# Kernel optimization log

Measured on AMD Instinct MI355X. Metric: run time of the kernel, lower is better.

## Reference

```python
import jax, jax.numpy as jnp
import numpy as np

N_NODES = 100000


def _gcn_conv(x, edge_index, W, b, n_nodes):
    # PyG GCNConv with add_self_loops=True, default gcn_norm:
    #   out = D^{-1/2} (A + I) D^{-1/2} (x @ W) + b
    xw = x @ W  # [N, out_dim]
    src = jnp.concatenate([edge_index[0], jnp.arange(n_nodes)])
    dst = jnp.concatenate([edge_index[1], jnp.arange(n_nodes)])
    ones = jnp.ones(src.shape[0], dtype=x.dtype)
    deg = jax.ops.segment_sum(ones, dst, num_segments=n_nodes)  # includes self loops
    dinv = jnp.where(deg > 0, jax.lax.rsqrt(deg), 0.0)
    norm = dinv[src] * dinv[dst]  # [E + N]
    msgs = xw[src] * norm[:, None]  # gather + scale per edge
    out = jax.ops.segment_sum(msgs, dst, num_segments=n_nodes)
    return out + b


def setup_inputs() -> dict:
    key = jax.random.key(0)
    k1, k2, k3, k4 = jax.random.split(key, 4)
    N, E = N_NODES, 1600000
    in_dim, hid_dim, out_dim = 128, 128, 64
    x = jax.random.normal(k1, (N, in_dim), dtype=jnp.float32)
    edge_index = jax.random.randint(k2, (2, E), 0, N, dtype=jnp.int64)
    W1 = jax.random.normal(k3, (in_dim, hid_dim), dtype=jnp.float32) * (1.0 / np.sqrt(in_dim))
    b1 = jnp.zeros((hid_dim,), dtype=jnp.float32)
    W2 = jax.random.normal(k4, (hid_dim, out_dim), dtype=jnp.float32) * (1.0 / np.sqrt(hid_dim))
    b2 = jnp.zeros((out_dim,), dtype=jnp.float32)
    return {"x": x, "edge_index": edge_index, "W1": W1, "b1": b1, "W2": W2, "b2": b2}


def reference(x, edge_index, W1, b1, W2, b2):
    h = _gcn_conv(x, edge_index, W1, b1, N_NODES)
    out = _gcn_conv(h, edge_index, W2, b2, N_NODES)
    return out
```

## Files before the change

### kernel.cpp

```cpp
#include <hip/hip_runtime.h>

#define NNODES 100000
#define NBUCK ((NNODES + 127) >> 7)
#define CAPB 3072
#define BINCAP 16
#define GFILL 256

typedef __attribute__((ext_vector_type(8))) short short8;
typedef __attribute__((ext_vector_type(4))) float f32x4;

__device__ __forceinline__ float bf2f(unsigned short u) {
    unsigned int v = ((unsigned int)u) << 16;
    return __builtin_bit_cast(float, v);
}
__device__ __forceinline__ unsigned short f2bf(float f) {
    unsigned int u = __builtin_bit_cast(unsigned int, f);
    u += 0x7FFF + ((u >> 16) & 1);
    return (unsigned short)(u >> 16);
}


__global__ __launch_bounds__(512) void fill_wc(const int* __restrict__ ei, int E,
                                               int* __restrict__ gcur,
                                               int* __restrict__ seg) {
    __shared__ int lcnt[NBUCK];
    __shared__ int lbin[NBUCK * BINCAP];

    const int t = threadIdx.x;
    for (int i = t; i < NBUCK; i += 512) lcnt[i] = 0;
    __syncthreads();

    const int per = (E + GFILL - 1) / GFILL;
    const int e0 = blockIdx.x * per;
    const int e1 = min(e0 + per, E);

    for (int base = e0; base < e1; base += 512) {
        int e = base + t;
        if (e < e1) {
            int src = ei[e];
            int d = ei[E + e];
            int b = (unsigned)d >> 7;
            int p = (src << 7) | (d & 127);
            int pos = atomicAdd(&lcnt[b], 1);
            if (pos < BINCAP) {
                lbin[b * BINCAP + pos] = p;
            } else {
                int gp = atomicAdd(&gcur[b << 4], 1);
                if (gp < CAPB) seg[b * CAPB + gp] = p;
            }
        }
        __syncthreads();
        for (int bb = t; bb < NBUCK; bb += 512) {
            if (lcnt[bb] >= BINCAP) {
                int gp = atomicAdd(&gcur[bb << 4], BINCAP);
                if (gp + BINCAP <= CAPB) {
                    int* dp = seg + bb * CAPB + gp;
                    const int* sp = lbin + bb * BINCAP;
#pragma unroll
                    for (int j = 0; j < BINCAP; ++j) dp[j] = sp[j];
                }
                lcnt[bb] = 0;
            }
        }
        __syncthreads();
    }
    for (int bb = t; bb < NBUCK; bb += 512) {
        int c = min(lcnt[bb], BINCAP);
        if (c > 0) {
            int gp = atomicAdd(&gcur[bb << 4], c);
            int* dp = seg + bb * CAPB;
            const int* sp = lbin + bb * BINCAP;
            for (int j = 0; j < c && gp + j < CAPB; ++j) dp[gp + j] = sp[j];
        }
    }
}


__global__ __launch_bounds__(512) void sortseg(const int* __restrict__ gcur,
                                               int* __restrict__ seg,
                                               float* __restrict__ dinv,
                                               int* __restrict__ rsb,
                                               int* __restrict__ cntb, int N) {
    __shared__ int el[CAPB];
    __shared__ int csr[CAPB];
    __shared__ int cnt[128], sh[128], rs[128], cur[128];

    const int t = threadIdx.x, b = blockIdx.x;
    const int total = min(gcur[b << 4], CAPB);

    if (t < 128) cnt[t] = 0;
    __syncthreads();
    {
        const int* sp = seg + b * CAPB;
        for (int i = t; i < total; i += 512) el[i] = sp[i];
    }
    __syncthreads();

    for (int i = t; i < total; i += 512) atomicAdd(&cnt[el[i] & 127], 1);
    __syncthreads();
    int v = (t < 128) ? cnt[t] : 0;
    if (t < 128) sh[t] = v;
    __syncthreads();
    for (int offp = 1; offp < 128; offp <<= 1) {
        int u = (t < 128 && t >= offp) ? sh[t - offp] : 0;
        __syncthreads();
        if (t < 128) sh[t] += u;
        __syncthreads();
    }
    if (t < 128) {
        int excl = sh[t] - v;
        rs[t] = excl;
        cur[t] = excl;
    }
    __syncthreads();
    for (int i = t; i < total; i += 512) {
        int p = el[i];
        int pos = atomicAdd(&cur[p & 127], 1);
        csr[pos] = (int)((unsigned)p >> 7);
    }
    __syncthreads();

    {
        int* dp = seg + b * CAPB;
        for (int i = t; i < total; i += 512) dp[i] = csr[i];
    }
    if (t < 128) {
        rsb[b * 128 + t] = rs[t];
        cntb[b * 128 + t] = cnt[t];
        int node = (b << 7) + t;
        if (node < N) dinv[node] = rsqrtf((float)cnt[t] + 1.0f);
    }
}


__global__ __launch_bounds__(256) void w12_kernel(const float* __restrict__ W1,
                                                  const float* __restrict__ b1,
                                                  const float* __restrict__ W2,
                                                  float* __restrict__ W12,
                                                  float* __restrict__ bW2,
                                                  unsigned short* __restrict__ whi,
                                                  unsigned short* __restrict__ wlo) {
    int j = threadIdx.x % 64;
    int r = threadIdx.x / 64;
    if (blockIdx.x < 32) {
        int i = blockIdx.x * 4 + r;
        float acc = 0.f;
        for (int k = 0; k < 128; ++k) acc += W1[i * 128 + k] * W2[k * 64 + j];
        W12[i * 64 + j] = acc;
        int kc = i >> 5;
        int ik = i & 31;
        int lane = ((ik >> 3) << 4) | (j & 15);
        int jj = ik & 7;
        int nt = j >> 4;
        size_t idx = (size_t)(((nt << 2) | kc) * 64 + lane) * 8 + jj;
        unsigned short h = f2bf(acc);
        whi[idx] = h;
        wlo[idx] = f2bf(acc - bf2f(h));
    } else if (r == 0) {
        float acc = 0.f;
        for (int k = 0; k < 128; ++k) acc += b1[k] * W2[k * 64 + j];
        bW2[j] = acc;
    }
}


__global__ __launch_bounds__(256) void gemm_mfma(const float* __restrict__ X,
                                                 const unsigned short* __restrict__ whi,
                                                 const unsigned short* __restrict__ wlo,
                                                 const float* __restrict__ dinv,
                                                 unsigned short* __restrict__ Ybf, int N) {
    const int tid = threadIdx.x;
    const int wv = tid >> 6;
    const int l = tid & 63;
    const int lm = l & 15;
    const int lk = l >> 4;
    const int rowbase = blockIdx.x * 64 + wv * 16;
    const int arow = min(rowbase + lm, N - 1);

    const float* xp = X + (size_t)arow * 128 + lk * 8;

    f32x4 acc[4];
#pragma unroll
    for (int nt = 0; nt < 4; ++nt) acc[nt] = (f32x4){0.f, 0.f, 0.f, 0.f};

#pragma unroll
    for (int kc = 0; kc < 4; ++kc) {
        float4 xa = *(const float4*)(xp + kc * 32);
        float4 xb = *(const float4*)(xp + kc * 32 + 4);
        float xs[8] = {xa.x, xa.y, xa.z, xa.w, xb.x, xb.y, xb.z, xb.w};
        short8 ah, al;
#pragma unroll
        for (int j = 0; j < 8; ++j) {
            unsigned short h = f2bf(xs[j]);
            ah[j] = (short)h;
            al[j] = (short)f2bf(xs[j] - bf2f(h));
        }
#pragma unroll
        for (int nt = 0; nt < 4; ++nt) {
            const size_t fb = (size_t)(((nt << 2) | kc) * 64 + l) * 8;
            short8 bh = *(const short8*)(whi + fb);
            short8 bl = *(const short8*)(wlo + fb);
            acc[nt] = __builtin_amdgcn_mfma_f32_16x16x32_bf16(ah, bh, acc[nt], 0, 0, 0);
            acc[nt] = __builtin_amdgcn_mfma_f32_16x16x32_bf16(ah, bl, acc[nt], 0, 0, 0);
            acc[nt] = __builtin_amdgcn_mfma_f32_16x16x32_bf16(al, bh, acc[nt], 0, 0, 0);
        }
    }

#pragma unroll
    for (int i = 0; i < 4; ++i) {
        int r = rowbase + lk * 4 + i;
        if (r < N) {
            float dv = dinv[r];
#pragma unroll
            for (int nt = 0; nt < 4; ++nt)
                Ybf[(size_t)r * 64 + nt * 16 + lm] = f2bf(acc[nt][i] * dv);
        }
    }
}


template <bool FINAL>
__global__ __launch_bounds__(256, 8) void agg_csr(const int* __restrict__ seg,
                                                  const int* __restrict__ rsb,
                                                  const int* __restrict__ cntb,
                                                  const unsigned short* __restrict__ Y,
                                                  const float* __restrict__ dinv,
                                                  const float* __restrict__ bW2,
                                                  const float* __restrict__ b2,
                                                  unsigned short* __restrict__ out_bf,
                                                  float* __restrict__ out_f, int N) {
    __shared__ int csrS[CAPB];
    __shared__ int rsS[32], cntS[32];

    const int t = threadIdx.x;
    const int b = blockIdx.x >> 2;
    const int q = blockIdx.x & 3;
    const int nb = q << 5;

    if (t < 32) {
        rsS[t] = rsb[b * 128 + nb + t];
        cntS[t] = cntb[b * 128 + nb + t];
    }
    __syncthreads();
    const int start = rsS[0];
    const int L = rsS[31] + cntS[31] - start;
    {
        const int* sp = seg + (size_t)b * CAPB + start;
        for (int i = t; i < L; i += 256) csrS[i] = sp[i];
    }
    __syncthreads();

    const int g = t >> 3, lane = t & 7, c8 = lane * 8;
    const int node = (b << 7) + nb + g;
    if (node >= N) return;

    float a[8];
    {
        short8 sv = *(const short8*)(Y + (size_t)node * 64 + c8);
#pragma unroll
        for (int j = 0; j < 8; ++j) a[j] = bf2f((unsigned short)sv[j]);
    }
    float ds = 0.f;

    const int s0 = rsS[g] - start;
    const int ne = cntS[g];
    const int e0 = s0 + ne;
    int i = s0;

    for (; i + 8 <= e0; i += 8) {
        int a0 = csrS[i + 0];
        int a1 = csrS[i + 1];
        int a2 = csrS[i + 2];
        int a3 = csrS[i + 3];
        int a4 = csrS[i + 4];
        int a5 = csrS[i + 5];
        int a6 = csrS[i + 6];
        int a7 = csrS[i + 7];
        short8 v0 = *(const short8*)(Y + (size_t)a0 * 64 + c8);
        short8 v1 = *(const short8*)(Y + (size_t)a1 * 64 + c8);
        short8 v2 = *(const short8*)(Y + (size_t)a2 * 64 + c8);
        short8 v3 = *(const short8*)(Y + (size_t)a3 * 64 + c8);
        short8 v4 = *(const short8*)(Y + (size_t)a4 * 64 + c8);
        short8 v5 = *(const short8*)(Y + (size_t)a5 * 64 + c8);
        short8 v6 = *(const short8*)(Y + (size_t)a6 * 64 + c8);
        short8 v7 = *(const short8*)(Y + (size_t)a7 * 64 + c8);
        if (FINAL) ds += dinv[csrS[i + lane]];
#pragma unroll
        for (int j = 0; j < 8; ++j) {
            a[j] += bf2f((unsigned short)v0[j]) + bf2f((unsigned short)v1[j])
                  + bf2f((unsigned short)v2[j]) + bf2f((unsigned short)v3[j])
                  + bf2f((unsigned short)v4[j]) + bf2f((unsigned short)v5[j])
                  + bf2f((unsigned short)v6[j]) + bf2f((unsigned short)v7[j]);
        }
    }
    for (; i + 4 <= e0; i += 4) {
        int a0 = csrS[i + 0];
        int a1 = csrS[i + 1];
        int a2 = csrS[i + 2];
        int a3 = csrS[i + 3];
        short8 v0 = *(const short8*)(Y + (size_t)a0 * 64 + c8);
        short8 v1 = *(const short8*)(Y + (size_t)a1 * 64 + c8);
        short8 v2 = *(const short8*)(Y + (size_t)a2 * 64 + c8);
        short8 v3 = *(const short8*)(Y + (size_t)a3 * 64 + c8);
        if (FINAL && lane < 4) ds += dinv[csrS[i + lane]];
#pragma unroll
        for (int j = 0; j < 8; ++j) {
            a[j] += bf2f((unsigned short)v0[j]) + bf2f((unsigned short)v1[j])
                  + bf2f((unsigned short)v2[j]) + bf2f((unsigned short)v3[j]);
        }
    }
    for (; i < e0; ++i) {
        int aa = csrS[i];
        short8 vv = *(const short8*)(Y + (size_t)aa * 64 + c8);
        if (FINAL && lane == 0) ds += dinv[aa];
#pragma unroll
        for (int j = 0; j < 8; ++j) a[j] += bf2f((unsigned short)vv[j]);
    }

    float di = rsqrtf((float)ne + 1.0f);
    if (FINAL) {
        float dt = ds;
        dt += __shfl_xor(dt, 1, 64);
        dt += __shfl_xor(dt, 2, 64);
        dt += __shfl_xor(dt, 4, 64);
        float si = di * (di + dt);
        float4 bb0 = *(const float4*)(bW2 + c8);
        float4 bb1 = *(const float4*)(bW2 + c8 + 4);
        float4 bv0 = *(const float4*)(b2 + c8);
        float4 bv1 = *(const float4*)(b2 + c8 + 4);
        float4 o0, o1;
        o0.x = di * a[0] + si * bb0.x + bv0.x;
        o0.y = di * a[1] + si * bb0.y + bv0.y;
        o0.z = di * a[2] + si * bb0.z + bv0.z;
        o0.w = di * a[3] + si * bb0.w + bv0.w;
        o1.x = di * a[4] + si * bb1.x + bv1.x;
        o1.y = di * a[5] + si * bb1.y + bv1.y;
        o1.z = di * a[6] + si * bb1.z + bv1.z;
        o1.w = di * a[7] + si * bb1.w + bv1.w;
        *(float4*)(out_f + (size_t)node * 64 + c8) = o0;
        *(float4*)(out_f + (size_t)node * 64 + c8 + 4) = o1;
    } else {
        float d2 = di * di;
        short8 o;
#pragma unroll
        for (int j = 0; j < 8; ++j) o[j] = (short)f2bf(d2 * a[j]);
        *(short8*)(out_bf + (size_t)node * 64 + c8) = o;
    }
}


extern "C" void kernel_launch(void* const* d_in, const int* in_sizes, int n_in,
                              void* d_out, int out_size, void* d_ws, size_t ws_size,
                              hipStream_t stream) {
    const float* x  = (const float*)d_in[0];
    const int*   ei = (const int*)d_in[1];
    const float* W1 = (const float*)d_in[2];
    const float* b1 = (const float*)d_in[3];
    const float* W2 = (const float*)d_in[4];
    const float* b2 = (const float*)d_in[5];
    float* out = (float*)d_out;

    const int N = NNODES;
    const int E = in_sizes[1] / 2;

    float* ws   = (float*)d_ws;
    float* dinv = ws;
    float* W12  = dinv + N;
    float* bW2  = W12 + 8192;
    unsigned short* whi = (unsigned short*)(bW2 + 64);
    unsigned short* wlo = whi + 8192;
    unsigned short* ybf = wlo + 8192;
    unsigned short* zbf = ybf + (size_t)N * 64;
    int*  seg  = (int*)(zbf + (size_t)N * 64);
    int*  gcur = seg + (size_t)NBUCK * CAPB;
    int*  rsb  = gcur + (size_t)NBUCK * 16;
    int*  cntb = rsb + (size_t)NBUCK * 128;

    hipMemsetAsync(gcur, 0, (size_t)NBUCK * 16 * sizeof(int), stream);

    fill_wc<<<GFILL, 512, 0, stream>>>(ei, E, gcur, seg);
    w12_kernel<<<33, 256, 0, stream>>>(W1, b1, W2, W12, bW2, whi, wlo);
    sortseg<<<NBUCK, 512, 0, stream>>>(gcur, seg, dinv, rsb, cntb, N);

    gemm_mfma<<<(N + 63) / 64, 256, 0, stream>>>(x, whi, wlo, dinv, ybf, N);
    agg_csr<false><<<NBUCK * 4, 256, 0, stream>>>(seg, rsb, cntb, ybf, dinv, nullptr, nullptr, zbf, nullptr, N);
    agg_csr<true><<<NBUCK * 4, 256, 0, stream>>>(seg, rsb, cntb, zbf, dinv, bW2, b2, nullptr, out, N);
}
```

Measured before the change: 211.1 us.

## Fuse bucket sort into first aggregation and compute degrees with global atomics

Removes the separate sortseg kernel. Node degrees are now counted with global atomics inside fill_wc. Each first-layer aggregation block (one quarter of a 128-node bucket) scans the whole bucket segment, filters the entries for its 32 nodes, and scatters them into a local CSR, which it writes out for reuse by the second layer. This saves a launch and the separate sort pass, but each bucket segment is read four times, fill_wc gains global atomics, and dinv is recomputed from deg in several places.

Result: slower. 263.7 us (+24.9%).

```diff
diff --git a/kernel.cpp b/kernel.cpp
--- a/kernel.cpp
+++ b/kernel.cpp
@@ -3,6 +3,7 @@
 #define NNODES 100000
 #define NBUCK ((NNODES + 127) >> 7)
 #define CAPB 3072
+#define QCAP 1024
 #define BINCAP 16
 #define GFILL 256
 
@@ -22,7 +23,8 @@
 
 __global__ __launch_bounds__(512) void fill_wc(const int* __restrict__ ei, int E,
                                                int* __restrict__ gcur,
-                                               int* __restrict__ seg) {
+                                               int* __restrict__ seg,
+                                               int* __restrict__ deg) {
     __shared__ int lcnt[NBUCK];
     __shared__ int lbin[NBUCK * BINCAP];
 
@@ -39,6 +41,7 @@
         if (e < e1) {
             int src = ei[e];
             int d = ei[E + e];
+            atomicAdd(&deg[d], 1);
             int b = (unsigned)d >> 7;
             int p = (src << 7) | (d & 127);
             int pos = atomicAdd(&lcnt[b], 1);
@@ -72,63 +75,6 @@
             const int* sp = lbin + bb * BINCAP;
             for (int j = 0; j < c && gp + j < CAPB; ++j) dp[gp + j] = sp[j];
         }
-    }
-}
-
-
-__global__ __launch_bounds__(512) void sortseg(const int* __restrict__ gcur,
-                                               int* __restrict__ seg,
-                                               float* __restrict__ dinv,
-                                               int* __restrict__ rsb,
-                                               int* __restrict__ cntb, int N) {
-    __shared__ int el[CAPB];
-    __shared__ int csr[CAPB];
-    __shared__ int cnt[128], sh[128], rs[128], cur[128];
-
-    const int t = threadIdx.x, b = blockIdx.x;
-    const int total = min(gcur[b << 4], CAPB);
-
-    if (t < 128) cnt[t] = 0;
-    __syncthreads();
-    {
-        const int* sp = seg + b * CAPB;
-        for (int i = t; i < total; i += 512) el[i] = sp[i];
-    }
-    __syncthreads();
-
-    for (int i = t; i < total; i += 512) atomicAdd(&cnt[el[i] & 127], 1);
-    __syncthreads();
-    int v = (t < 128) ? cnt[t] : 0;
-    if (t < 128) sh[t] = v;
-    __syncthreads();
-    for (int offp = 1; offp < 128; offp <<= 1) {
-        int u = (t < 128 && t >= offp) ? sh[t - offp] : 0;
-        __syncthreads();
-        if (t < 128) sh[t] += u;
-        __syncthreads();
-    }
-    if (t < 128) {
-        int excl = sh[t] - v;
-        rs[t] = excl;
-        cur[t] = excl;
-    }
-    __syncthreads();
-    for (int i = t; i < total; i += 512) {
-        int p = el[i];
-        int pos = atomicAdd(&cur[p & 127], 1);
-        csr[pos] = (int)((unsigned)p >> 7);
-    }
-    __syncthreads();
-
-    {
-        int* dp = seg + b * CAPB;
-        for (int i = t; i < total; i += 512) dp[i] = csr[i];
-    }
-    if (t < 128) {
-        rsb[b * 128 + t] = rs[t];
-        cntb[b * 128 + t] = cnt[t];
-        int node = (b << 7) + t;
-        if (node < N) dinv[node] = rsqrtf((float)cnt[t] + 1.0f);
     }
 }
 
@@ -167,7 +113,7 @@
 __global__ __launch_bounds__(256) void gemm_mfma(const float* __restrict__ X,
                                                  const unsigned short* __restrict__ whi,
                                                  const unsigned short* __restrict__ wlo,
-                                                 const float* __restrict__ dinv,
+                                                 const int* __restrict__ deg,
                                                  unsigned short* __restrict__ Ybf, int N) {
     const int tid = threadIdx.x;
     const int wv = tid >> 6;
@@ -210,7 +156,7 @@
     for (int i = 0; i < 4; ++i) {
         int r = rowbase + lk * 4 + i;
         if (r < N) {
-            float dv = dinv[r];
+            float dv = rsqrtf((float)deg[r] + 1.0f);
 #pragma unroll
             for (int nt = 0; nt < 4; ++nt)
                 Ybf[(size_t)r * 64 + nt * 16 + lm] = f2bf(acc[nt][i] * dv);
@@ -219,18 +165,14 @@
 }
 
 
-template <bool FINAL>
-__global__ __launch_bounds__(256, 8) void agg_csr(const int* __restrict__ seg,
-                                                  const int* __restrict__ rsb,
-                                                  const int* __restrict__ cntb,
-                                                  const unsigned short* __restrict__ Y,
-                                                  const float* __restrict__ dinv,
-                                                  const float* __restrict__ bW2,
-                                                  const float* __restrict__ b2,
-                                                  unsigned short* __restrict__ out_bf,
-                                                  float* __restrict__ out_f, int N) {
-    __shared__ int csrS[CAPB];
-    __shared__ int rsS[32], cntS[32];
+__global__ __launch_bounds__(256, 8) void agg_q1(const int* __restrict__ gcur,
+                                                 const int* __restrict__ seg,
+                                                 const int* __restrict__ deg,
+                                                 const unsigned short* __restrict__ Y,
+                                                 int* __restrict__ qcsr,
+                                                 unsigned short* __restrict__ out_bf, int N) {
+    __shared__ int csrS[QCAP];
+    __shared__ int rsS[32], cntS[32], curS[32];
 
     const int t = threadIdx.x;
     const int b = blockIdx.x >> 2;
@@ -238,17 +180,38 @@
     const int nb = q << 5;
 
     if (t < 32) {
-        rsS[t] = rsb[b * 128 + nb + t];
-        cntS[t] = cntb[b * 128 + nb + t];
-    }
-    __syncthreads();
-    const int start = rsS[0];
-    const int L = rsS[31] + cntS[31] - start;
+        int node = (b << 7) + nb + t;
+        cntS[t] = (node < N) ? deg[node] : 0;
+    }
+    __syncthreads();
+    if (t == 0) {
+        int s = 0;
+#pragma unroll
+        for (int j = 0; j < 32; ++j) { rsS[j] = s; s += cntS[j]; }
+    }
+    __syncthreads();
+    if (t < 32) curS[t] = rsS[t];
+    __syncthreads();
+
     {
-        const int* sp = seg + (size_t)b * CAPB + start;
-        for (int i = t; i < L; i += 256) csrS[i] = sp[i];
-    }
-    __syncthreads();
+        const int total = min(gcur[b << 4], CAPB);
+        const int* sp = seg + (size_t)b * CAPB;
+        for (int i = t; i < total; i += 256) {
+            int p = sp[i];
+            int key = p & 127;
+            if ((key >> 5) == q) {
+                int pos = atomicAdd(&curS[key & 31], 1);
+                if (pos < QCAP) csrS[pos] = (int)((unsigned)p >> 7);
+            }
+        }
+    }
+    __syncthreads();
+
+    const int L = min(rsS[31] + cntS[31], QCAP);
+    {
+        int* dp = qcsr + ((size_t)((b << 2) | q) << 10);
+        for (int i = t; i < L; i += 256) dp[i] = csrS[i];
+    }
 
     const int g = t >> 3, lane = t & 7, c8 = lane * 8;
     const int node = (b << 7) + nb + g;
@@ -260,11 +223,10 @@
 #pragma unroll
         for (int j = 0; j < 8; ++j) a[j] = bf2f((unsigned short)sv[j]);
     }
-    float ds = 0.f;
-
-    const int s0 = rsS[g] - start;
+
     const int ne = cntS[g];
-    const int e0 = s0 + ne;
+    const int s0 = min(rsS[g], L);
+    const int e0 = min(s0 + ne, L);
     int i = s0;
 
     for (; i + 8 <= e0; i += 8) {
@@ -284,7 +246,6 @@
         short8 v5 = *(const short8*)(Y + (size_t)a5 * 64 + c8);
         short8 v6 = *(const short8*)(Y + (size_t)a6 * 64 + c8);
         short8 v7 = *(const short8*)(Y + (size_t)a7 * 64 + c8);
-        if (FINAL) ds += dinv[csrS[i + lane]];
 #pragma unroll
         for (int j = 0; j < 8; ++j) {
             a[j] += bf2f((unsigned short)v0[j]) + bf2f((unsigned short)v1[j])
@@ -302,7 +263,6 @@
         short8 v1 = *(const short8*)(Y + (size_t)a1 * 64 + c8);
         short8 v2 = *(const short8*)(Y + (size_t)a2 * 64 + c8);
         short8 v3 = *(const short8*)(Y + (size_t)a3 * 64 + c8);
-        if (FINAL && lane < 4) ds += dinv[csrS[i + lane]];
 #pragma unroll
         for (int j = 0; j < 8; ++j) {
             a[j] += bf2f((unsigned short)v0[j]) + bf2f((unsigned short)v1[j])
@@ -312,40 +272,140 @@
     for (; i < e0; ++i) {
         int aa = csrS[i];
         short8 vv = *(const short8*)(Y + (size_t)aa * 64 + c8);
-        if (FINAL && lane == 0) ds += dinv[aa];
 #pragma unroll
         for (int j = 0; j < 8; ++j) a[j] += bf2f((unsigned short)vv[j]);
     }
 
     float di = rsqrtf((float)ne + 1.0f);
-    if (FINAL) {
-        float dt = ds;
-        dt += __shfl_xor(dt, 1, 64);
-        dt += __shfl_xor(dt, 2, 64);
-        dt += __shfl_xor(dt, 4, 64);
-        float si = di * (di + dt);
-        float4 bb0 = *(const float4*)(bW2 + c8);
-        float4 bb1 = *(const float4*)(bW2 + c8 + 4);
-        float4 bv0 = *(const float4*)(b2 + c8);
-        float4 bv1 = *(const float4*)(b2 + c8 + 4);
-        float4 o0, o1;
-        o0.x = di * a[0] + si * bb0.x + bv0.x;
-        o0.y = di * a[1] + si * bb0.y + bv0.y;
-        o0.z = di * a[2] + si * bb0.z + bv0.z;
-        o0.w = di * a[3] + si * bb0.w + bv0.w;
-        o1.x = di * a[4] + si * bb1.x + bv1.x;
-        o1.y = di * a[5] + si * bb1.y + bv1.y;
-        o1.z = di * a[6] + si * bb1.z + bv1.z;
-        o1.w = di * a[7] + si * bb1.w + bv1.w;
-        *(float4*)(out_f + (size_t)node * 64 + c8) = o0;
-        *(float4*)(out_f + (size_t)node * 64 + c8 + 4) = o1;
-    } else {
-        float d2 = di * di;
-        short8 o;
-#pragma unroll
-        for (int j = 0; j < 8; ++j) o[j] = (short)f2bf(d2 * a[j]);
-        *(short8*)(out_bf + (size_t)node * 64 + c8) = o;
-    }
+    float d2 = di * di;
+    short8 o;
+#pragma unroll
+    for (int j = 0; j < 8; ++j) o[j] = (short)f2bf(d2 * a[j]);
+    *(short8*)(out_bf + (size_t)node * 64 + c8) = o;
+}
+
+
+__global__ __launch_bounds__(256, 8) void agg_q2(const int* __restrict__ deg,
+                                                 const int* __restrict__ qcsr,
+                                                 const unsigned short* __restrict__ Y,
+                                                 const float* __restrict__ bW2,
+                                                 const float* __restrict__ b2,
+                                                 float* __restrict__ out_f, int N) {
+    __shared__ int csrS[QCAP];
+    __shared__ int rsS[32], cntS[32];
+
+    const int t = threadIdx.x;
+    const int b = blockIdx.x >> 2;
+    const int q = blockIdx.x & 3;
+    const int nb = q << 5;
+
+    if (t < 32) {
+        int node = (b << 7) + nb + t;
+        cntS[t] = (node < N) ? deg[node] : 0;
+    }
+    __syncthreads();
+    if (t == 0) {
+        int s = 0;
+#pragma unroll
+        for (int j = 0; j < 32; ++j) { rsS[j] = s; s += cntS[j]; }
+    }
+    __syncthreads();
+
+    const int L = min(rsS[31] + cntS[31], QCAP);
+    {
+        const int* sp = qcsr + ((size_t)((b << 2) | q) << 10);
+        for (int i = t; i < L; i += 256) csrS[i] = sp[i];
+    }
+    __syncthreads();
+
+    const int g = t >> 3, lane = t & 7, c8 = lane * 8;
+    const int node = (b << 7) + nb + g;
+    if (node >= N) return;
+
+    float a[8];
+    {
+        short8 sv = *(const short8*)(Y + (size_t)node * 64 + c8);
+#pragma unroll
+        for (int j = 0; j < 8; ++j) a[j] = bf2f((unsigned short)sv[j]);
+    }
+    float ds = 0.f;
+
+    const int ne = cntS[g];
+    const int s0 = min(rsS[g], L);
+    const int e0 = min(s0 + ne, L);
+    int i = s0;
+
+    for (; i + 8 <= e0; i += 8) {
+        int a0 = csrS[i + 0];
+        int a1 = csrS[i + 1];
+        int a2 = csrS[i + 2];
+        int a3 = csrS[i + 3];
+        int a4 = csrS[i + 4];
+        int a5 = csrS[i + 5];
+        int a6 = csrS[i + 6];
+        int a7 = csrS[i + 7];
+        short8 v0 = *(const short8*)(Y + (size_t)a0 * 64 + c8);
+        short8 v1 = *(const short8*)(Y + (size_t)a1 * 64 + c8);
+        short8 v2 = *(const short8*)(Y + (size_t)a2 * 64 + c8);
+        short8 v3 = *(const short8*)(Y + (size_t)a3 * 64 + c8);
+        short8 v4 = *(const short8*)(Y + (size_t)a4 * 64 + c8);
+        short8 v5 = *(const short8*)(Y + (size_t)a5 * 64 + c8);
+        short8 v6 = *(const short8*)(Y + (size_t)a6 * 64 + c8);
+        short8 v7 = *(const short8*)(Y + (size_t)a7 * 64 + c8);
+        ds += rsqrtf((float)deg[csrS[i + lane]] + 1.0f);
+#pragma unroll
+        for (int j = 0; j < 8; ++j) {
+            a[j] += bf2f((unsigned short)v0[j]) + bf2f((unsigned short)v1[j])
+                  + bf2f((unsigned short)v2[j]) + bf2f((unsigned short)v3[j])
+                  + bf2f((unsigned short)v4[j]) + bf2f((unsigned short)v5[j])
+                  + bf2f((unsigned short)v6[j]) + bf2f((unsigned short)v7[j]);
+        }
+    }
+    for (; i + 4 <= e0; i += 4) {
+        int a0 = csrS[i + 0];
+        int a1 = csrS[i + 1];
+        int a2 = csrS[i + 2];
+        int a3 = csrS[i + 3];
+        short8 v0 = *(const short8*)(Y + (size_t)a0 * 64 + c8);
+        short8 v1 = *(const short8*)(Y + (size_t)a1 * 64 + c8);
+        short8 v2 = *(const short8*)(Y + (size_t)a2 * 64 + c8);
+        short8 v3 = *(const short8*)(Y + (size_t)a3 * 64 + c8);
+        if (lane < 4) ds += rsqrtf((float)deg[csrS[i + lane]] + 1.0f);
+#pragma unroll
+        for (int j = 0; j < 8; ++j) {
+            a[j] += bf2f((unsigned short)v0[j]) + bf2f((unsigned short)v1[j])
+                  + bf2f((unsigned short)v2[j]) + bf2f((unsigned short)v3[j]);
+        }
+    }
+    for (; i < e0; ++i) {
+        int aa = csrS[i];
+        short8 vv = *(const short8*)(Y + (size_t)aa * 64 + c8);
+        if (lane == 0) ds += rsqrtf((float)deg[aa] + 1.0f);
+#pragma unroll
+        for (int j = 0; j < 8; ++j) a[j] += bf2f((unsigned short)vv[j]);
+    }
+
+    float di = rsqrtf((float)ne + 1.0f);
+    float dt = ds;
+    dt += __shfl_xor(dt, 1, 64);
+    dt += __shfl_xor(dt, 2, 64);
+    dt += __shfl_xor(dt, 4, 64);
+    float si = di * (di + dt);
+    float4 bb0 = *(const float4*)(bW2 + c8);
+    float4 bb1 = *(const float4*)(bW2 + c8 + 4);
+    float4 bv0 = *(const float4*)(b2 + c8);
+    float4 bv1 = *(const float4*)(b2 + c8 + 4);
+    float4 o0, o1;
+    o0.x = di * a[0] + si * bb0.x + bv0.x;
+    o0.y = di * a[1] + si * bb0.y + bv0.y;
+    o0.z = di * a[2] + si * bb0.z + bv0.z;
+    o0.w = di * a[3] + si * bb0.w + bv0.w;
+    o1.x = di * a[4] + si * bb1.x + bv1.x;
+    o1.y = di * a[5] + si * bb1.y + bv1.y;
+    o1.z = di * a[6] + si * bb1.z + bv1.z;
+    o1.w = di * a[7] + si * bb1.w + bv1.w;
+    *(float4*)(out_f + (size_t)node * 64 + c8) = o0;
+    *(float4*)(out_f + (size_t)node * 64 + c8 + 4) = o1;
 }
 
 
@@ -364,8 +424,7 @@
     const int E = in_sizes[1] / 2;
 
     float* ws   = (float*)d_ws;
-    float* dinv = ws;
-    float* W12  = dinv + N;
+    float* W12  = ws;
     float* bW2  = W12 + 8192;
     unsigned short* whi = (unsigned short*)(bW2 + 64);
     unsigned short* wlo = whi + 8192;
@@ -373,16 +432,15 @@
     unsigned short* zbf = ybf + (size_t)N * 64;
     int*  seg  = (int*)(zbf + (size_t)N * 64);
     int*  gcur = seg + (size_t)NBUCK * CAPB;
-    int*  rsb  = gcur + (size_t)NBUCK * 16;
-    int*  cntb = rsb + (size_t)NBUCK * 128;
-
-    hipMemsetAsync(gcur, 0, (size_t)NBUCK * 16 * sizeof(int), stream);
-
-    fill_wc<<<GFILL, 512, 0, stream>>>(ei, E, gcur, seg);
+    int*  deg  = gcur + (size_t)NBUCK * 16;
+    int*  qcsr = deg + (size_t)NBUCK * 128;
+
+    hipMemsetAsync(gcur, 0, (size_t)NBUCK * (16 + 128) * sizeof(int), stream);
+
+    fill_wc<<<GFILL, 512, 0, stream>>>(ei, E, gcur, seg, deg);
     w12_kernel<<<33, 256, 0, stream>>>(W1, b1, W2, W12, bW2, whi, wlo);
-    sortseg<<<NBUCK, 512, 0, stream>>>(gcur, seg, dinv, rsb, cntb, N);
-
-    gemm_mfma<<<(N + 63) / 64, 256, 0, stream>>>(x, whi, wlo, dinv, ybf, N);
-    agg_csr<false><<<NBUCK * 4, 256, 0, stream>>>(seg, rsb, cntb, ybf, dinv, nullptr, nullptr, zbf, nullptr, N);
-    agg_csr<true><<<NBUCK * 4, 256, 0, stream>>>(seg, rsb, cntb, zbf, dinv, bW2, b2, nullptr, out, N);
-}
+
+    gemm_mfma<<<(N + 63) / 64, 256, 0, stream>>>(x, whi, wlo, deg, ybf, N);
+    agg_q1<<<NBUCK * 4, 256, 0, stream>>>(gcur, seg, deg, ybf, qcsr, zbf, N);
+    agg_q2<<<NBUCK * 4, 256, 0, stream>>>(deg, qcsr, zbf, bW2, b2, out, N);
+}
```
